# Optimization experiments

Hardware: AMD Instinct MI355X
Metric: run time of the kernel (lower is better)

Reference implementation:

```python
import jax, jax.numpy as jnp
import numpy as np

B, NPG = 128, 128          # graphs, nodes per graph
N = B * NPG                # total nodes
K = 16                     # kNN neighbors within cutoff
D = 256                    # embedding_depth
H, DH = 4, 32              # heads = num_layers, head dim = (D//2)//H
L = 4                      # num graph convolutions
NR = 50                    # num_radial
CUTOFF = 2.0
OUT = 3 + 100              # 3 + max_ntypes


def setup_inputs() -> dict:
    rng = np.random.default_rng(0)
    pos = rng.standard_normal((N, 3)).astype(np.float32)
    nbrs = np.zeros((N, K), np.int32)
    mask = np.zeros((N, K), np.float32)
    for g in range(B):  # per-graph kNN with radial cutoff (setup only, numpy)
        p = pos[g * NPG:(g + 1) * NPG]
        d2 = ((p[:, None, :] - p[None, :, :]) ** 2).sum(-1)
        np.fill_diagonal(d2, np.inf)
        idx = np.argsort(d2, axis=1)[:, :K]
        dk = np.sqrt(np.take_along_axis(d2, idx, 1))
        nbrs[g * NPG:(g + 1) * NPG] = idx + g * NPG
        mask[g * NPG:(g + 1) * NPG] = (dk <= CUTOFF).astype(np.float32)
    batch_idx = np.repeat(np.arange(B, dtype=np.int32), NPG)

    key = jax.random.key(0)
    ks = jax.random.split(key, 12)
    s = 0.02
    return {
        'encoding': jax.random.normal(ks[0], (B, D), jnp.float32),
        'pos': jnp.asarray(pos),
        'batch_idx': jnp.asarray(batch_idx),
        'neighbors': jnp.asarray(nbrs),
        'nbr_mask': jnp.asarray(mask),
        'W_in': jax.random.normal(ks[1], (D + 3, D), jnp.float32) * s,
        'b_in': jnp.zeros((D,), jnp.float32),
        'Wq': jax.random.normal(ks[2], (L, D, H * DH), jnp.float32) * s,
        'Wk': jax.random.normal(ks[3], (L, D, H * DH), jnp.float32) * s,
        'Wv': jax.random.normal(ks[4], (L, D, H * DH), jnp.float32) * s,
        'We': jax.random.normal(ks[5], (L, NR, H * DH), jnp.float32) * s,
        'Wo': jax.random.normal(ks[6], (L, H * DH, D), jnp.float32) * s,
        'bo': jnp.zeros((L, D), jnp.float32),
        'Wfc': jax.random.normal(ks[7], (L, D, D), jnp.float32) * s,
        'bfc': jnp.zeros((L, D), jnp.float32),
        'ln_g': jnp.ones((L, D), jnp.float32),
        'ln_b': jnp.zeros((L, D), jnp.float32),
        'W_out': jax.random.normal(ks[8], (D, OUT), jnp.float32) * s,
        'b_out': jnp.zeros((OUT,), jnp.float32),
    }


def reference(encoding, pos, batch_idx, neighbors, nbr_mask,
              W_in, b_in, Wq, Wk, Wv, We, Wo, bo, Wfc, bfc,
              ln_g, ln_b, W_out, b_out):
    # x = encoding.repeat_interleave(graph_sizes); x[:, 0] = 1
    x = encoding[batch_idx]                      # [N, D]
    x = x.at[:, 0].set(1.0)
    h = jnp.concatenate([x, pos], axis=-1) @ W_in + b_in   # concat pos, embed

    # gaussian radial basis of neighbor distances
    dvec = pos[neighbors] - pos[:, None, :]      # [N, K, 3]
    d = jnp.sqrt((dvec ** 2).sum(-1) + 1e-12)    # [N, K]
    centers = jnp.linspace(0.0, CUTOFF, NR)
    width = centers[1] - centers[0]
    rbf = jnp.exp(-0.5 * ((d[..., None] - centers) / width) ** 2)  # [N, K, NR]

    scale = 1.0 / jnp.sqrt(jnp.float32(DH))
    m = nbr_mask[..., None]                      # [N, K, 1]
    for l in range(L):                           # TransformerConv layers
        q = (h @ Wq[l]).reshape(N, H, DH)
        k = (h @ Wk[l]).reshape(N, H, DH)
        v = (h @ Wv[l]).reshape(N, H, DH)
        e = (rbf @ We[l]).reshape(N, K, H, DH)   # edge embedding
        kj = k[neighbors] + e                    # [N, K, H, DH]
        vj = v[neighbors] + e
        logits = jnp.einsum('nhd,nkhd->nkh', q, kj) * scale
        logits = jnp.where(m > 0, logits, -1e9)
        a = jax.nn.softmax(logits, axis=1) * m   # masked attention over K
        msg = jnp.einsum('nkh,nkhd->nhd', a, vj).reshape(N, H * DH)
        h = h + msg @ Wo[l] + bo[l]              # residual update
        mu = h.mean(-1, keepdims=True)
        var = h.var(-1, keepdims=True)
        h = ln_g[l] * (h - mu) / jnp.sqrt(var + 1e-5) + ln_b[l]
        h = jax.nn.gelu(h @ Wfc[l] + bfc[l])     # nodewise fc (1 layer)

    return h @ W_out + b_out                     # [N, 3 + max_ntypes]
```

## Files before the change

### kernel.cpp

```cpp
#include <hip/hip_runtime.h>
#include <hip/hip_bf16.h>
#include <math.h>

#define N_PTS 16384
#define NLAYER 4

typedef __attribute__((ext_vector_type(8))) short bfrag;
typedef __attribute__((ext_vector_type(4))) float f32x4;
typedef unsigned short ushort_t;
typedef unsigned int uint_t;

__device__ __forceinline__ ushort_t f2b(float f) {
  __hip_bfloat16 h = __float2bfloat16(f);
  return *reinterpret_cast<const ushort_t*>(&h);
}
__device__ __forceinline__ float b2f(ushort_t u) {
  union { uint_t i; float f; } c; c.i = ((uint_t)u) << 16; return c.f;
}
__device__ __forceinline__ float blo(uint_t u) {
  union { uint_t i; float f; } c; c.i = u << 16; return c.f;
}
__device__ __forceinline__ float bhi(uint_t u) {
  union { uint_t i; float f; } c; c.i = u & 0xffff0000u; return c.f;
}

__global__ __launch_bounds__(256) void base_kernel(
    const float* __restrict__ enc, const float* __restrict__ W_in,
    const float* __restrict__ b_in, float* __restrict__ base)
{
  int b = blockIdx.x, j = threadIdx.x;
  __shared__ float se[256];
  se[j] = enc[b * 256 + j];
  __syncthreads();
  float acc = b_in[j] + W_in[j];
  for (int i = 1; i < 256; ++i) acc += se[i] * W_in[i * 256 + j];
  base[b * 256 + j] = acc;
}

__global__ __launch_bounds__(256) void embed_kernel(
    const float* __restrict__ base, const int* __restrict__ batch_idx,
    const float* __restrict__ pos, const float* __restrict__ W_in,
    float* __restrict__ h, ushort_t* __restrict__ h_bf)
{
  int n = blockIdx.x, j = threadIdx.x;
  int b = batch_idx[n];
  float px = pos[n * 3 + 0], py = pos[n * 3 + 1], pz = pos[n * 3 + 2];
  float v = base[b * 256 + j]
      + px * W_in[256 * 256 + j] + py * W_in[257 * 256 + j] + pz * W_in[258 * 256 + j];
  h[(size_t)n * 256 + j] = v;
  h_bf[(size_t)n * 256 + j] = f2b(v);
}

__global__ __launch_bounds__(256) void prep_qkv(
    const float* __restrict__ Wq, const float* __restrict__ Wk,
    const float* __restrict__ Wv, const float* __restrict__ We,
    ushort_t* __restrict__ out)
{
  int idx = blockIdx.x * 256 + threadIdx.x;
  int l = idx / (640 * 256);
  int rem = idx - l * (640 * 256);
  int j = rem >> 8, k = rem & 255;
  float v = 0.f;
  if (j < 128) v = Wq[((size_t)l * 256 + k) * 128 + j];
  else if (j < 328) {
    int p = j - 128, hq = p / 50, r = p - hq * 50;
    const float* wq = &Wq[((size_t)l * 256 + k) * 128 + hq * 32];
    const float* we = &We[((size_t)l * 50 + r) * 128 + hq * 32];
#pragma unroll
    for (int d = 0; d < 32; ++d) v += wq[d] * we[d];
  } else if (j < 456) v = Wk[((size_t)l * 256 + k) * 128 + (j - 328)];
  else if (j < 584) v = Wv[((size_t)l * 256 + k) * 128 + (j - 456)];
  out[idx] = f2b(v);
}

__global__ __launch_bounds__(256) void prep_bcat(
    const float* __restrict__ We, const float* __restrict__ Wo, ushort_t* __restrict__ out)
{
  int idx = blockIdx.x * 256 + threadIdx.x;
  int l = idx / (256 * 384);
  int rem = idx - l * (256 * 384);
  int j = rem / 384, k2 = rem - j * 384;
  float v = 0.f;
  if (k2 < 128) v = Wo[((size_t)l * 128 + k2) * 256 + j];
  else if (k2 < 328) {
    int p = k2 - 128, hq = p / 50, r = p - hq * 50;
    const float* we = &We[((size_t)l * 50 + r) * 128 + hq * 32];
    const float* wo = &Wo[((size_t)l * 128 + hq * 32) * 256 + j];
#pragma unroll
    for (int d = 0; d < 32; ++d) v += we[d] * wo[(size_t)d * 256];
  }
  out[idx] = f2b(v);
}

__global__ __launch_bounds__(256) void prep_wfc(
    const float* __restrict__ Wfc, ushort_t* __restrict__ out)
{
  int idx = blockIdx.x * 256 + threadIdx.x;
  int l = idx >> 16, rem = idx & 65535;
  int j = rem >> 8, k = rem & 255;
  out[idx] = f2b(Wfc[((size_t)l * 256 + k) * 256 + j]);
}

__global__ __launch_bounds__(256) void prep_wout(
    const float* __restrict__ W_out, ushort_t* __restrict__ out)
{
  int idx = blockIdx.x * 256 + threadIdx.x;
  int j = idx >> 8, k = idx & 255;
  out[idx] = (j < 103) ? f2b(W_out[(size_t)k * 103 + j]) : (ushort_t)0;
}

template<int MODE>
__global__ __launch_bounds__(256, 3) void fused_layer(
    const ushort_t* __restrict__ A0,
    const ushort_t* __restrict__ BcT,
    const float* __restrict__ bo,
    float* __restrict__ h,
    const float* __restrict__ lg, const float* __restrict__ lb,
    const ushort_t* __restrict__ WfT,
    const float* __restrict__ bfc,
    const ushort_t* __restrict__ W3T,
    const float* __restrict__ b3,
    ushort_t* __restrict__ qext_b, ushort_t* __restrict__ kvb,
    float* __restrict__ outF)
{
  __shared__ __align__(16) ushort_t sA[32 * 392];
  __shared__ __align__(16) ushort_t sH[32 * 264];
  __shared__ float pS[4][32], pSS[4][32];

  const int tid = threadIdx.x;
  const int lane = tid & 63, w = tid >> 6;
  const int l15 = lane & 15, l4 = lane >> 4;
  const int m0 = blockIdx.x * 32;

  if constexpr (MODE != 2) {
    for (int i = tid; i < 32 * 44; i += 256) {
      int r = i / 44, c8 = i - r * 44;
      *(uint4*)(&sA[r * 392 + c8 * 8]) =
          *(const uint4*)(A0 + (size_t)(m0 + r) * 352 + c8 * 8);
    }
    __syncthreads();

    const int c_0 = w * 64 + l15, c_1 = c_0 + 16, c_2 = c_0 + 32, c_3 = c_0 + 48;

    f32x4 acc[2][4];
#pragma unroll
    for (int m = 0; m < 2; ++m)
#pragma unroll
      for (int nn = 0; nn < 4; ++nn) acc[m][nn] = (f32x4){0.f, 0.f, 0.f, 0.f};
    {
      const ushort_t* bp0 = BcT + (size_t)(c_0) * 384 + l4 * 8;
      const ushort_t* bp1 = BcT + (size_t)(c_1) * 384 + l4 * 8;
      const ushort_t* bp2 = BcT + (size_t)(c_2) * 384 + l4 * 8;
      const ushort_t* bp3 = BcT + (size_t)(c_3) * 384 + l4 * 8;
#pragma unroll
      for (int k0 = 0; k0 < 352; k0 += 32) {
        bfrag a0 = *(const bfrag*)(sA + l15 * 392 + k0 + l4 * 8);
        bfrag a1 = *(const bfrag*)(sA + (16 + l15) * 392 + k0 + l4 * 8);
        bfrag b0 = *(const bfrag*)(bp0 + k0);
        bfrag b1 = *(const bfrag*)(bp1 + k0);
        bfrag b2 = *(const bfrag*)(bp2 + k0);
        bfrag b3v = *(const bfrag*)(bp3 + k0);
        __builtin_amdgcn_s_setprio(1);
        acc[0][0] = __builtin_amdgcn_mfma_f32_16x16x32_bf16(a0, b0, acc[0][0], 0, 0, 0);
        acc[0][1] = __builtin_amdgcn_mfma_f32_16x16x32_bf16(a0, b1, acc[0][1], 0, 0, 0);
        acc[0][2] = __builtin_amdgcn_mfma_f32_16x16x32_bf16(a0, b2, acc[0][2], 0, 0, 0);
        acc[0][3] = __builtin_amdgcn_mfma_f32_16x16x32_bf16(a0, b3v, acc[0][3], 0, 0, 0);
        acc[1][0] = __builtin_amdgcn_mfma_f32_16x16x32_bf16(a1, b0, acc[1][0], 0, 0, 0);
        acc[1][1] = __builtin_amdgcn_mfma_f32_16x16x32_bf16(a1, b1, acc[1][1], 0, 0, 0);
        acc[1][2] = __builtin_amdgcn_mfma_f32_16x16x32_bf16(a1, b2, acc[1][2], 0, 0, 0);
        acc[1][3] = __builtin_amdgcn_mfma_f32_16x16x32_bf16(a1, b3v, acc[1][3], 0, 0, 0);
        __builtin_amdgcn_s_setprio(0);
      }
    }

    {
      const float bo_[4] = {bo[c_0], bo[c_1], bo[c_2], bo[c_3]};
#pragma unroll
      for (int m = 0; m < 2; ++m)
#pragma unroll
        for (int i = 0; i < 4; ++i) {
          const int rl = m * 16 + l4 * 4 + i;
          const size_t r = (size_t)(m0 + rl);
          float x0 = acc[m][0][i] + bo_[0] + h[r * 256 + c_0];
          float x1 = acc[m][1][i] + bo_[1] + h[r * 256 + c_1];
          float x2 = acc[m][2][i] + bo_[2] + h[r * 256 + c_2];
          float x3 = acc[m][3][i] + bo_[3] + h[r * 256 + c_3];
          acc[m][0][i] = x0; acc[m][1][i] = x1;
          acc[m][2][i] = x2; acc[m][3][i] = x3;
          float s = x0 + x1 + x2 + x3;
          float ss = x0 * x0 + x1 * x1 + x2 * x2 + x3 * x3;
          s += __shfl_xor(s, 1, 64); ss += __shfl_xor(ss, 1, 64);
          s += __shfl_xor(s, 2, 64); ss += __shfl_xor(ss, 2, 64);
          s += __shfl_xor(s, 4, 64); ss += __shfl_xor(ss, 4, 64);
          s += __shfl_xor(s, 8, 64); ss += __shfl_xor(ss, 8, 64);
          if (l15 == 0) { pS[w][rl] = s; pSS[w][rl] = ss; }
        }
    }
    __syncthreads();
    {
      const float lg_[4] = {lg[c_0], lg[c_1], lg[c_2], lg[c_3]};
      const float lb_[4] = {lb[c_0], lb[c_1], lb[c_2], lb[c_3]};
#pragma unroll
      for (int m = 0; m < 2; ++m)
#pragma unroll
        for (int i = 0; i < 4; ++i) {
          const int rl = m * 16 + l4 * 4 + i;
          float s = pS[0][rl] + pS[1][rl] + pS[2][rl] + pS[3][rl];
          float ss = pSS[0][rl] + pSS[1][rl] + pSS[2][rl] + pSS[3][rl];
          float mu = s * (1.f / 256.f);
          float var = ss * (1.f / 256.f) - mu * mu;
          float inv = 1.0f / sqrtf(var + 1e-5f);
          sH[rl * 264 + c_0] = f2b(lg_[0] * (acc[m][0][i] - mu) * inv + lb_[0]);
          sH[rl * 264 + c_1] = f2b(lg_[1] * (acc[m][1][i] - mu) * inv + lb_[1]);
          sH[rl * 264 + c_2] = f2b(lg_[2] * (acc[m][2][i] - mu) * inv + lb_[2]);
          sH[rl * 264 + c_3] = f2b(lg_[3] * (acc[m][3][i] - mu) * inv + lb_[3]);
        }
    }
    __syncthreads();

#pragma unroll
    for (int m = 0; m < 2; ++m)
#pragma unroll
      for (int nn = 0; nn < 4; ++nn) acc[m][nn] = (f32x4){0.f, 0.f, 0.f, 0.f};
    {
      const ushort_t* bp0 = WfT + (size_t)(c_0) * 256 + l4 * 8;
      const ushort_t* bp1 = WfT + (size_t)(c_1) * 256 + l4 * 8;
      const ushort_t* bp2 = WfT + (size_t)(c_2) * 256 + l4 * 8;
      const ushort_t* bp3 = WfT + (size_t)(c_3) * 256 + l4 * 8;
#pragma unroll
      for (int k0 = 0; k0 < 256; k0 += 32) {
        bfrag a0 = *(const bfrag*)(sH + l15 * 264 + k0 + l4 * 8);
        bfrag a1 = *(const bfrag*)(sH + (16 + l15) * 264 + k0 + l4 * 8);
        bfrag b0 = *(const bfrag*)(bp0 + k0);
        bfrag b1 = *(const bfrag*)(bp1 + k0);
        bfrag b2 = *(const bfrag*)(bp2 + k0);
        bfrag b3v = *(const bfrag*)(bp3 + k0);
        __builtin_amdgcn_s_setprio(1);
        acc[0][0] = __builtin_amdgcn_mfma_f32_16x16x32_bf16(a0, b0, acc[0][0], 0, 0, 0);
        acc[0][1] = __builtin_amdgcn_mfma_f32_16x16x32_bf16(a0, b1, acc[0][1], 0, 0, 0);
        acc[0][2] = __builtin_amdgcn_mfma_f32_16x16x32_bf16(a0, b2, acc[0][2], 0, 0, 0);
        acc[0][3] = __builtin_amdgcn_mfma_f32_16x16x32_bf16(a0, b3v, acc[0][3], 0, 0, 0);
        acc[1][0] = __builtin_amdgcn_mfma_f32_16x16x32_bf16(a1, b0, acc[1][0], 0, 0, 0);
        acc[1][1] = __builtin_amdgcn_mfma_f32_16x16x32_bf16(a1, b1, acc[1][1], 0, 0, 0);
        acc[1][2] = __builtin_amdgcn_mfma_f32_16x16x32_bf16(a1, b2, acc[1][2], 0, 0, 0);
        acc[1][3] = __builtin_amdgcn_mfma_f32_16x16x32_bf16(a1, b3v, acc[1][3], 0, 0, 0);
        __builtin_amdgcn_s_setprio(0);
      }
    }

    {
      const float bf_[4] = {bfc[c_0], bfc[c_1], bfc[c_2], bfc[c_3]};
      const int cc[4] = {c_0, c_1, c_2, c_3};
#pragma unroll
      for (int m = 0; m < 2; ++m)
#pragma unroll
        for (int i = 0; i < 4; ++i) {
          const int rl = m * 16 + l4 * 4 + i;
          const size_t r = (size_t)(m0 + rl);
#pragma unroll
          for (int nn = 0; nn < 4; ++nn) {
            float x = acc[m][nn][i] + bf_[nn];
            float t = tanhf(0.7978845608028654f * (x + 0.044715f * x * x * x));
            float gl = 0.5f * x * (1.f + t);
            h[r * 256 + cc[nn]] = gl;
            sA[rl * 264 + cc[nn]] = f2b(gl);
          }
        }
    }
    __syncthreads();
  } else {
    for (int i = tid; i < 32 * 32; i += 256) {
      int r = i >> 5, c8 = i & 31;
      *(uint4*)(&sA[r * 264 + c8 * 8]) =
          *(const uint4*)(A0 + (size_t)(m0 + r) * 256 + c8 * 8);
    }
    __syncthreads();
  }

  const int NPAN = (MODE == 1) ? 2 : 10;
  const int WCOL = (MODE == 1) ? 32 : 160;
  for (int p = 0; p < NPAN; ++p) {
    const int cb = w * WCOL + p * 16;
    const int c = cb + l15;
    const ushort_t* bp = W3T + (size_t)c * 256 + l4 * 8;
    f32x4 aA[2], aB[2];
    aA[0] = (f32x4){0.f, 0.f, 0.f, 0.f}; aA[1] = aA[0];
    aB[0] = aA[0]; aB[1] = aA[0];
#pragma unroll
    for (int k0 = 0; k0 < 128; k0 += 32) {
      bfrag a0 = *(const bfrag*)(sA + l15 * 264 + k0 + l4 * 8);
      bfrag a1 = *(const bfrag*)(sA + (16 + l15) * 264 + k0 + l4 * 8);
      bfrag b0 = *(const bfrag*)(bp + k0);
      __builtin_amdgcn_s_setprio(1);
      aA[0] = __builtin_amdgcn_mfma_f32_16x16x32_bf16(a0, b0, aA[0], 0, 0, 0);
      aA[1] = __builtin_amdgcn_mfma_f32_16x16x32_bf16(a1, b0, aA[1], 0, 0, 0);
      __builtin_amdgcn_s_setprio(0);
    }
#pragma unroll
    for (int k0 = 128; k0 < 256; k0 += 32) {
      bfrag a0 = *(const bfrag*)(sA + l15 * 264 + k0 + l4 * 8);
      bfrag a1 = *(const bfrag*)(sA + (16 + l15) * 264 + k0 + l4 * 8);
      bfrag b0 = *(const bfrag*)(bp + k0);
      __builtin_amdgcn_s_setprio(1);
      aB[0] = __builtin_amdgcn_mfma_f32_16x16x32_bf16(a0, b0, aB[0], 0, 0, 0);
      aB[1] = __builtin_amdgcn_mfma_f32_16x16x32_bf16(a1, b0, aB[1], 0, 0, 0);
      __builtin_amdgcn_s_setprio(0);
    }
#pragma unroll
    for (int m = 0; m < 2; ++m)
#pragma unroll
      for (int i = 0; i < 4; ++i) {
        const size_t r = (size_t)(m0 + m * 16 + l4 * 4 + i);
        float v = aA[m][i] + aB[m][i];
        if constexpr (MODE == 1) {
          if (c < 103) outF[r * 103 + c] = v + b3[c];
        } else {
          if (c < 328) qext_b[r * 352 + c] = f2b(v);
          else if (c < 584) kvb[r * 256 + (c - 328)] = f2b(v);
        }
      }
  }
}

__global__ __launch_bounds__(256) void attn_kernel(
    const ushort_t* __restrict__ qext, const ushort_t* __restrict__ kvb,
    const float* __restrict__ pos, const int* __restrict__ nbrs,
    const float* __restrict__ mask, ushort_t* __restrict__ Amsg)
{
  __shared__ __align__(16) ushort_t sQ[4][128];
  __shared__ __align__(16) float    sQE[4][4][52];
  __shared__ __align__(16) ushort_t sRbf[4][16][52];
  __shared__ float sA[4][64];
  __shared__ float sD[4][16];
  __shared__ float sMk[4][16];
  __shared__ int   sNb[4][16];

  const int tid = threadIdx.x;
  const int lane = tid & 63, w = tid >> 6;
  const int g = blockIdx.x & 127, q4 = blockIdx.x >> 7;
  const int kk = lane >> 2, hh = lane & 3;

  for (int it = 0; it < 4; ++it) {
    const int n = g * 128 + q4 * 16 + w * 4 + it;
    if (lane < 16) {
      int nb = nbrs[n * 16 + lane];
      sNb[w][lane] = nb;
      sMk[w][lane] = mask[n * 16 + lane];
      float dx = pos[nb * 3 + 0] - pos[n * 3 + 0];
      float dy = pos[nb * 3 + 1] - pos[n * 3 + 1];
      float dz = pos[nb * 3 + 2] - pos[n * 3 + 2];
      sD[w][lane] = sqrtf(dx * dx + dy * dy + dz * dz + 1e-12f);
      sRbf[w][lane][50] = 0; sRbf[w][lane][51] = 0;
      *(uint4*)(&sQ[w][lane * 8]) = *(const uint4*)(qext + (size_t)n * 352 + lane * 8);
    }
    if (lane < 50) {
      uint2 u = *(const uint2*)(qext + (size_t)n * 352 + 128 + lane * 4);
      int p = lane * 4;
#pragma unroll
      for (int e = 0; e < 4; ++e) {
        ushort_t bb = ((const ushort_t*)&u)[e];
        int pp = p + e, h2 = pp / 50, r = pp - h2 * 50;
        sQE[w][h2][r] = b2f(bb);
      }
    }
    if (lane < 8) sQE[w][lane >> 1][50 + (lane & 1)] = 0.f;
    {
      int kk2 = lane & 15;
      float dk = sD[w][kk2];
      int r0 = lane >> 4;
#pragma unroll
      for (int j = 0; j < 13; ++j) {
        int r = r0 + j * 4;
        if (r < 50) {
          float t = (dk - (2.f / 49.f) * (float)r) * 24.5f;
          sRbf[w][kk2][r] = f2b(__expf(-0.5f * t * t));
        }
      }
    }
    const int nb = sNb[w][kk];
    const ushort_t* krow = kvb + (size_t)nb * 256 + hh * 32;
    float qk = 0.f;
#pragma unroll
    for (int c8 = 0; c8 < 4; ++c8) {
      uint4 kv4 = *(const uint4*)(krow + c8 * 8);
      const uint_t* q4p = (const uint_t*)(&sQ[w][hh * 32 + c8 * 8]);
      uint_t qa = q4p[0], qb = q4p[1], qc = q4p[2], qd = q4p[3];
      qk += blo(qa) * blo(kv4.x) + bhi(qa) * bhi(kv4.x)
          + blo(qb) * blo(kv4.y) + bhi(qb) * bhi(kv4.y)
          + blo(qc) * blo(kv4.z) + bhi(qc) * bhi(kv4.z)
          + blo(qd) * blo(kv4.w) + bhi(qd) * bhi(kv4.w);
    }
    float qe = 0.f;
#pragma unroll
    for (int c = 0; c < 13; ++c) {
      float4 qv = *(const float4*)(&sQE[w][hh][c * 4]);
      uint2 rv = *(const uint2*)(&sRbf[w][kk][c * 4]);
      qe += qv.x * blo(rv.x) + qv.y * bhi(rv.x)
          + qv.z * blo(rv.y) + qv.w * bhi(rv.y);
    }
    float lg = 0.17677669529663687f * (qk + qe);
    lg = (sMk[w][kk] > 0.f) ? lg : -1e9f;

    float mx = lg;
#pragma unroll
    for (int off = 4; off < 64; off <<= 1) mx = fmaxf(mx, __shfl_xor(mx, off, 64));
    float ex = __expf(lg - mx);
    float sm = ex;
#pragma unroll
    for (int off = 4; off < 64; off <<= 1) sm += __shfl_xor(sm, off, 64);
    sA[w][kk * 4 + hh] = ex / sm * sMk[w][kk];

    if (lane < 50) {
      float r0 = 0.f, r1 = 0.f, r2 = 0.f, r3 = 0.f;
#pragma unroll
      for (int k2 = 0; k2 < 16; ++k2) {
        float rb = b2f(sRbf[w][k2][lane]);
        r0 += sA[w][k2 * 4 + 0] * rb;
        r1 += sA[w][k2 * 4 + 1] * rb;
        r2 += sA[w][k2 * 4 + 2] * rb;
        r3 += sA[w][k2 * 4 + 3] * rb;
      }
      Amsg[(size_t)n * 352 + 128 + 0 * 50 + lane] = f2b(r0);
      Amsg[(size_t)n * 352 + 128 + 1 * 50 + lane] = f2b(r1);
      Amsg[(size_t)n * 352 + 128 + 2 * 50 + lane] = f2b(r2);
      Amsg[(size_t)n * 352 + 128 + 3 * 50 + lane] = f2b(r3);
    }
    {
      const int h2 = lane >> 4;
      float m0v = 0.f, m1v = 0.f;
#pragma unroll
      for (int k2 = 0; k2 < 16; ++k2) {
        int nb2 = sNb[w][k2];
        uint_t vv = *(const uint_t*)(kvb + (size_t)nb2 * 256 + 128 + lane * 2);
        float a = sA[w][k2 * 4 + h2];
        m0v += a * blo(vv);
        m1v += a * bhi(vv);
      }
      uint_t o = (uint_t)f2b(m0v) | ((uint_t)f2b(m1v) << 16);
      *(uint_t*)(&Amsg[(size_t)n * 352 + lane * 2]) = o;
    }
    if (lane < 24) Amsg[(size_t)n * 352 + 328 + lane] = 0;
  }
}

extern "C" void kernel_launch(void* const* d_in, const int* in_sizes, int n_in,
                              void* d_out, int out_size, void* d_ws, size_t ws_size,
                              hipStream_t stream) {
  const float* enc    = (const float*)d_in[0];
  const float* pos    = (const float*)d_in[1];
  const int*   bidx   = (const int*)  d_in[2];
  const int*   nbrs   = (const int*)  d_in[3];
  const float* mask   = (const float*)d_in[4];
  const float* W_in   = (const float*)d_in[5];
  const float* b_in   = (const float*)d_in[6];
  const float* Wq     = (const float*)d_in[7];
  const float* Wk     = (const float*)d_in[8];
  const float* Wv     = (const float*)d_in[9];
  const float* We     = (const float*)d_in[10];
  const float* Wo     = (const float*)d_in[11];
  const float* bo     = (const float*)d_in[12];
  const float* Wfc    = (const float*)d_in[13];
  const float* bfc    = (const float*)d_in[14];
  const float* ln_g   = (const float*)d_in[15];
  const float* ln_b   = (const float*)d_in[16];
  const float* W_out  = (const float*)d_in[17];
  const float* b_out  = (const float*)d_in[18];
  float* out = (float*)d_out;

  const int N = N_PTS;
  float* ws = (float*)d_ws;
  float*    h      = ws;
  ushort_t* qext_b = (ushort_t*)(h + (size_t)N * 256);
  ushort_t* kvb    = qext_b + (size_t)N * 352;
  ushort_t* h_bf   = kvb + (size_t)N * 256;
  ushort_t* Amsg   = h_bf + (size_t)N * 256;
  float*    base   = (float*)(Amsg + (size_t)N * 352);
  ushort_t* WqkvT  = (ushort_t*)(base + 128 * 256);
  ushort_t* BcT    = WqkvT + 4 * 640 * 256;
  ushort_t* WfT    = BcT  + 4 * 256 * 384;
  ushort_t* WoT    = WfT  + 4 * 256 * 256;

  base_kernel<<<128, 256, 0, stream>>>(enc, W_in, b_in, base);
  embed_kernel<<<N, 256, 0, stream>>>(base, bidx, pos, W_in, h, h_bf);
  prep_qkv<<<(4 * 640 * 256) / 256, 256, 0, stream>>>(Wq, Wk, Wv, We, WqkvT);
  prep_bcat<<<(4 * 256 * 384) / 256, 256, 0, stream>>>(We, Wo, BcT);
  prep_wfc<<<(4 * 256 * 256) / 256, 256, 0, stream>>>(Wfc, WfT);
  prep_wout<<<(128 * 256) / 256, 256, 0, stream>>>(W_out, WoT);

  fused_layer<2><<<N / 32, 256, 0, stream>>>(
      h_bf, nullptr, nullptr, nullptr, nullptr, nullptr, nullptr, nullptr,
      WqkvT, nullptr, qext_b, kvb, nullptr);

  for (int l = 0; l < NLAYER; ++l) {
    const ushort_t* BcT_l = BcT + (size_t)l * 256 * 384;
    const ushort_t* WfT_l = WfT + (size_t)l * 256 * 256;
    const float* bo_l  = bo  + (size_t)l * 256;
    const float* bfc_l = bfc + (size_t)l * 256;
    const float* lg_l  = ln_g + (size_t)l * 256;
    const float* lb_l  = ln_b + (size_t)l * 256;

    attn_kernel<<<1024, 256, 0, stream>>>(qext_b, kvb, pos, nbrs, mask, Amsg);

    if (l < NLAYER - 1) {
      const ushort_t* Wqkv_next = WqkvT + (size_t)(l + 1) * 640 * 256;
      fused_layer<0><<<N / 32, 256, 0, stream>>>(
          Amsg, BcT_l, bo_l, h, lg_l, lb_l, WfT_l, bfc_l,
          Wqkv_next, nullptr, qext_b, kvb, nullptr);
    } else {
      fused_layer<1><<<N / 32, 256, 0, stream>>>(
          Amsg, BcT_l, bo_l, h, lg_l, lb_l, WfT_l, bfc_l,
          WoT, b_out, nullptr, nullptr, out);
    }
  }
}
```

Baseline: 387.0 us.

## Retile fused layer warps to 2x2 row/column split with register-prefetched operands

Reorganizes the fused layer so each warp owns 16 rows by 128 columns, reading the A operand straight from global memory instead of staging it in shared memory. B fragments are double-buffered in registers so the next k-step's loads overlap the current MFMAs. The QKV/output projection panel loop becomes a strided tile loop over 16-column tiles with two tiles in flight. Occupancy hint drops from 3 to 2 blocks per CU to make room for the larger register footprint, and the output weight prep is widened to 144 rows to cover the padded tile count.

Result: slower. 469.7 us (+21.4%).

```diff
diff --git a/kernel.cpp b/kernel.cpp
--- a/kernel.cpp
+++ b/kernel.cpp
@@ -23,6 +23,8 @@
 __device__ __forceinline__ float bhi(uint_t u) {
   union { uint_t i; float f; } c; c.i = u & 0xffff0000u; return c.f;
 }
+
+#define MFMA16(a, b, c) __builtin_amdgcn_mfma_f32_16x16x32_bf16((a), (b), (c), 0, 0, 0)
 
 __global__ __launch_bounds__(256) void base_kernel(
     const float* __restrict__ enc, const float* __restrict__ W_in,
@@ -105,12 +107,13 @@
     const float* __restrict__ W_out, ushort_t* __restrict__ out)
 {
   int idx = blockIdx.x * 256 + threadIdx.x;
+  if (idx >= 144 * 256) return;
   int j = idx >> 8, k = idx & 255;
   out[idx] = (j < 103) ? f2b(W_out[(size_t)k * 103 + j]) : (ushort_t)0;
 }
 
 template<int MODE>
-__global__ __launch_bounds__(256, 3) void fused_layer(
+__global__ __launch_bounds__(256, 2) void fused_layer(
     const ushort_t* __restrict__ A0,
     const ushort_t* __restrict__ BcT,
     const float* __restrict__ bo,
@@ -123,202 +126,189 @@
     ushort_t* __restrict__ qext_b, ushort_t* __restrict__ kvb,
     float* __restrict__ outF)
 {
-  __shared__ __align__(16) ushort_t sA[32 * 392];
   __shared__ __align__(16) ushort_t sH[32 * 264];
-  __shared__ float pS[4][32], pSS[4][32];
+  __shared__ __align__(16) ushort_t sG[32 * 264];
+  __shared__ float pS[2][32], pSS[2][32];
 
   const int tid = threadIdx.x;
   const int lane = tid & 63, w = tid >> 6;
+  const int rh = w >> 1, ch = w & 1;
   const int l15 = lane & 15, l4 = lane >> 4;
   const int m0 = blockIdx.x * 32;
+  const int arow = rh * 16 + l15;
 
   if constexpr (MODE != 2) {
-    for (int i = tid; i < 32 * 44; i += 256) {
-      int r = i / 44, c8 = i - r * 44;
-      *(uint4*)(&sA[r * 392 + c8 * 8]) =
-          *(const uint4*)(A0 + (size_t)(m0 + r) * 352 + c8 * 8);
+    const int cbase = ch * 128;
+
+    f32x4 acc[8];
+#pragma unroll
+    for (int nt = 0; nt < 8; ++nt) acc[nt] = (f32x4){0.f, 0.f, 0.f, 0.f};
+    {
+      const ushort_t* ap = A0 + (size_t)(m0 + arow) * 352 + l4 * 8;
+      const ushort_t* bp[8];
+#pragma unroll
+      for (int nt = 0; nt < 8; ++nt)
+        bp[nt] = BcT + (size_t)(cbase + nt * 16 + l15) * 384 + l4 * 8;
+      bfrag aC = *(const bfrag*)ap;
+      bfrag bC[8];
+#pragma unroll
+      for (int nt = 0; nt < 8; ++nt) bC[nt] = *(const bfrag*)bp[nt];
+#pragma unroll
+      for (int ks = 0; ks < 11; ++ks) {
+        bfrag aN{}; bfrag bN[8];
+        if (ks < 10) {
+          aN = *(const bfrag*)(ap + (ks + 1) * 32);
+#pragma unroll
+          for (int nt = 0; nt < 8; ++nt) bN[nt] = *(const bfrag*)(bp[nt] + (ks + 1) * 32);
+        }
+        __builtin_amdgcn_s_setprio(1);
+#pragma unroll
+        for (int nt = 0; nt < 8; ++nt) acc[nt] = MFMA16(aC, bC[nt], acc[nt]);
+        __builtin_amdgcn_s_setprio(0);
+        if (ks < 10) {
+          aC = aN;
+#pragma unroll
+          for (int nt = 0; nt < 8; ++nt) bC[nt] = bN[nt];
+        }
+      }
+    }
+
+    {
+#pragma unroll
+      for (int i = 0; i < 4; ++i) {
+        const int rl = rh * 16 + l4 * 4 + i;
+        const size_t r = (size_t)(m0 + rl);
+        float s = 0.f, ss = 0.f;
+#pragma unroll
+        for (int nt = 0; nt < 8; ++nt) {
+          const int c = cbase + nt * 16 + l15;
+          float x = acc[nt][i] + bo[c] + h[r * 256 + c];
+          acc[nt][i] = x;
+          s += x; ss += x * x;
+        }
+        s += __shfl_xor(s, 1, 64); ss += __shfl_xor(ss, 1, 64);
+        s += __shfl_xor(s, 2, 64); ss += __shfl_xor(ss, 2, 64);
+        s += __shfl_xor(s, 4, 64); ss += __shfl_xor(ss, 4, 64);
+        s += __shfl_xor(s, 8, 64); ss += __shfl_xor(ss, 8, 64);
+        if (l15 == 0) { pS[ch][rl] = s; pSS[ch][rl] = ss; }
+      }
     }
     __syncthreads();
-
-    const int c_0 = w * 64 + l15, c_1 = c_0 + 16, c_2 = c_0 + 32, c_3 = c_0 + 48;
-
-    f32x4 acc[2][4];
-#pragma unroll
-    for (int m = 0; m < 2; ++m)
-#pragma unroll
-      for (int nn = 0; nn < 4; ++nn) acc[m][nn] = (f32x4){0.f, 0.f, 0.f, 0.f};
-    {
-      const ushort_t* bp0 = BcT + (size_t)(c_0) * 384 + l4 * 8;
-      const ushort_t* bp1 = BcT + (size_t)(c_1) * 384 + l4 * 8;
-      const ushort_t* bp2 = BcT + (size_t)(c_2) * 384 + l4 * 8;
-      const ushort_t* bp3 = BcT + (size_t)(c_3) * 384 + l4 * 8;
-#pragma unroll
-      for (int k0 = 0; k0 < 352; k0 += 32) {
-        bfrag a0 = *(const bfrag*)(sA + l15 * 392 + k0 + l4 * 8);
-        bfrag a1 = *(const bfrag*)(sA + (16 + l15) * 392 + k0 + l4 * 8);
-        bfrag b0 = *(const bfrag*)(bp0 + k0);
-        bfrag b1 = *(const bfrag*)(bp1 + k0);
-        bfrag b2 = *(const bfrag*)(bp2 + k0);
-        bfrag b3v = *(const bfrag*)(bp3 + k0);
+    {
+#pragma unroll
+      for (int i = 0; i < 4; ++i) {
+        const int rl = rh * 16 + l4 * 4 + i;
+        float s = pS[0][rl] + pS[1][rl];
+        float ss = pSS[0][rl] + pSS[1][rl];
+        float mu = s * (1.f / 256.f);
+        float var = ss * (1.f / 256.f) - mu * mu;
+        float inv = 1.0f / sqrtf(var + 1e-5f);
+#pragma unroll
+        for (int nt = 0; nt < 8; ++nt) {
+          const int c = cbase + nt * 16 + l15;
+          sH[rl * 264 + c] = f2b(lg[c] * (acc[nt][i] - mu) * inv + lb[c]);
+        }
+      }
+    }
+    __syncthreads();
+
+#pragma unroll
+    for (int nt = 0; nt < 8; ++nt) acc[nt] = (f32x4){0.f, 0.f, 0.f, 0.f};
+    {
+      const ushort_t* bp[8];
+#pragma unroll
+      for (int nt = 0; nt < 8; ++nt)
+        bp[nt] = WfT + (size_t)(cbase + nt * 16 + l15) * 256 + l4 * 8;
+      bfrag bC[8];
+#pragma unroll
+      for (int nt = 0; nt < 8; ++nt) bC[nt] = *(const bfrag*)bp[nt];
+#pragma unroll
+      for (int ks = 0; ks < 8; ++ks) {
+        bfrag bN[8];
+        if (ks < 7) {
+#pragma unroll
+          for (int nt = 0; nt < 8; ++nt) bN[nt] = *(const bfrag*)(bp[nt] + (ks + 1) * 32);
+        }
+        bfrag aC = *(const bfrag*)(sH + arow * 264 + ks * 32 + l4 * 8);
         __builtin_amdgcn_s_setprio(1);
-        acc[0][0] = __builtin_amdgcn_mfma_f32_16x16x32_bf16(a0, b0, acc[0][0], 0, 0, 0);
-        acc[0][1] = __builtin_amdgcn_mfma_f32_16x16x32_bf16(a0, b1, acc[0][1], 0, 0, 0);
-        acc[0][2] = __builtin_amdgcn_mfma_f32_16x16x32_bf16(a0, b2, acc[0][2], 0, 0, 0);
-        acc[0][3] = __builtin_amdgcn_mfma_f32_16x16x32_bf16(a0, b3v, acc[0][3], 0, 0, 0);
-        acc[1][0] = __builtin_amdgcn_mfma_f32_16x16x32_bf16(a1, b0, acc[1][0], 0, 0, 0);
-        acc[1][1] = __builtin_amdgcn_mfma_f32_16x16x32_bf16(a1, b1, acc[1][1], 0, 0, 0);
-        acc[1][2] = __builtin_amdgcn_mfma_f32_16x16x32_bf16(a1, b2, acc[1][2], 0, 0, 0);
-        acc[1][3] = __builtin_amdgcn_mfma_f32_16x16x32_bf16(a1, b3v, acc[1][3], 0, 0, 0);
+#pragma unroll
+        for (int nt = 0; nt < 8; ++nt) acc[nt] = MFMA16(aC, bC[nt], acc[nt]);
         __builtin_amdgcn_s_setprio(0);
-      }
-    }
-
-    {
-      const float bo_[4] = {bo[c_0], bo[c_1], bo[c_2], bo[c_3]};
-#pragma unroll
-      for (int m = 0; m < 2; ++m)
-#pragma unroll
-        for (int i = 0; i < 4; ++i) {
-          const int rl = m * 16 + l4 * 4 + i;
-          const size_t r = (size_t)(m0 + rl);
-          float x0 = acc[m][0][i] + bo_[0] + h[r * 256 + c_0];
-          float x1 = acc[m][1][i] + bo_[1] + h[r * 256 + c_1];
-          float x2 = acc[m][2][i] + bo_[2] + h[r * 256 + c_2];
-          float x3 = acc[m][3][i] + bo_[3] + h[r * 256 + c_3];
-          acc[m][0][i] = x0; acc[m][1][i] = x1;
-          acc[m][2][i] = x2; acc[m][3][i] = x3;
-          float s = x0 + x1 + x2 + x3;
-          float ss = x0 * x0 + x1 * x1 + x2 * x2 + x3 * x3;
-          s += __shfl_xor(s, 1, 64); ss += __shfl_xor(ss, 1, 64);
-          s += __shfl_xor(s, 2, 64); ss += __shfl_xor(ss, 2, 64);
-          s += __shfl_xor(s, 4, 64); ss += __shfl_xor(ss, 4, 64);
-          s += __shfl_xor(s, 8, 64); ss += __shfl_xor(ss, 8, 64);
-          if (l15 == 0) { pS[w][rl] = s; pSS[w][rl] = ss; }
-        }
-    }
-    __syncthreads();
-    {
-      const float lg_[4] = {lg[c_0], lg[c_1], lg[c_2], lg[c_3]};
-      const float lb_[4] = {lb[c_0], lb[c_1], lb[c_2], lb[c_3]};
-#pragma unroll
-      for (int m = 0; m < 2; ++m)
-#pragma unroll
-        for (int i = 0; i < 4; ++i) {
-          const int rl = m * 16 + l4 * 4 + i;
-          float s = pS[0][rl] + pS[1][rl] + pS[2][rl] + pS[3][rl];
-          float ss = pSS[0][rl] + pSS[1][rl] + pSS[2][rl] + pSS[3][rl];
-          float mu = s * (1.f / 256.f);
-          float var = ss * (1.f / 256.f) - mu * mu;
-          float inv = 1.0f / sqrtf(var + 1e-5f);
-          sH[rl * 264 + c_0] = f2b(lg_[0] * (acc[m][0][i] - mu) * inv + lb_[0]);
-          sH[rl * 264 + c_1] = f2b(lg_[1] * (acc[m][1][i] - mu) * inv + lb_[1]);
-          sH[rl * 264 + c_2] = f2b(lg_[2] * (acc[m][2][i] - mu) * inv + lb_[2]);
-          sH[rl * 264 + c_3] = f2b(lg_[3] * (acc[m][3][i] - mu) * inv + lb_[3]);
-        }
-    }
-    __syncthreads();
-
-#pragma unroll
-    for (int m = 0; m < 2; ++m)
-#pragma unroll
-      for (int nn = 0; nn < 4; ++nn) acc[m][nn] = (f32x4){0.f, 0.f, 0.f, 0.f};
-    {
-      const ushort_t* bp0 = WfT + (size_t)(c_0) * 256 + l4 * 8;
-      const ushort_t* bp1 = WfT + (size_t)(c_1) * 256 + l4 * 8;
-      const ushort_t* bp2 = WfT + (size_t)(c_2) * 256 + l4 * 8;
-      const ushort_t* bp3 = WfT + (size_t)(c_3) * 256 + l4 * 8;
-#pragma unroll
-      for (int k0 = 0; k0 < 256; k0 += 32) {
-        bfrag a0 = *(const bfrag*)(sH + l15 * 264 + k0 + l4 * 8);
-        bfrag a1 = *(const bfrag*)(sH + (16 + l15) * 264 + k0 + l4 * 8);
-        bfrag b0 = *(const bfrag*)(bp0 + k0);
-        bfrag b1 = *(const bfrag*)(bp1 + k0);
-        bfrag b2 = *(const bfrag*)(bp2 + k0);
-        bfrag b3v = *(const bfrag*)(bp3 + k0);
-        __builtin_amdgcn_s_setprio(1);
-        acc[0][0] = __builtin_amdgcn_mfma_f32_16x16x32_bf16(a0, b0, acc[0][0], 0, 0, 0);
-        acc[0][1] = __builtin_amdgcn_mfma_f32_16x16x32_bf16(a0, b1, acc[0][1], 0, 0, 0);
-        acc[0][2] = __builtin_amdgcn_mfma_f32_16x16x32_bf16(a0, b2, acc[0][2], 0, 0, 0);
-        acc[0][3] = __builtin_amdgcn_mfma_f32_16x16x32_bf16(a0, b3v, acc[0][3], 0, 0, 0);
-        acc[1][0] = __builtin_amdgcn_mfma_f32_16x16x32_bf16(a1, b0, acc[1][0], 0, 0, 0);
-        acc[1][1] = __builtin_amdgcn_mfma_f32_16x16x32_bf16(a1, b1, acc[1][1], 0, 0, 0);
-        acc[1][2] = __builtin_amdgcn_mfma_f32_16x16x32_bf16(a1, b2, acc[1][2], 0, 0, 0);
-        acc[1][3] = __builtin_amdgcn_mfma_f32_16x16x32_bf16(a1, b3v, acc[1][3], 0, 0, 0);
-        __builtin_amdgcn_s_setprio(0);
-      }
-    }
-
-    {
-      const float bf_[4] = {bfc[c_0], bfc[c_1], bfc[c_2], bfc[c_3]};
-      const int cc[4] = {c_0, c_1, c_2, c_3};
-#pragma unroll
-      for (int m = 0; m < 2; ++m)
-#pragma unroll
-        for (int i = 0; i < 4; ++i) {
-          const int rl = m * 16 + l4 * 4 + i;
-          const size_t r = (size_t)(m0 + rl);
-#pragma unroll
-          for (int nn = 0; nn < 4; ++nn) {
-            float x = acc[m][nn][i] + bf_[nn];
-            float t = tanhf(0.7978845608028654f * (x + 0.044715f * x * x * x));
-            float gl = 0.5f * x * (1.f + t);
-            h[r * 256 + cc[nn]] = gl;
-            sA[rl * 264 + cc[nn]] = f2b(gl);
-          }
-        }
+        if (ks < 7) {
+#pragma unroll
+          for (int nt = 0; nt < 8; ++nt) bC[nt] = bN[nt];
+        }
+      }
+    }
+
+    {
+#pragma unroll
+      for (int i = 0; i < 4; ++i) {
+        const int rl = rh * 16 + l4 * 4 + i;
+        const size_t r = (size_t)(m0 + rl);
+#pragma unroll
+        for (int nt = 0; nt < 8; ++nt) {
+          const int c = cbase + nt * 16 + l15;
+          float x = acc[nt][i] + bfc[c];
+          float t = tanhf(0.7978845608028654f * (x + 0.044715f * x * x * x));
+          float gl = 0.5f * x * (1.f + t);
+          h[r * 256 + c] = gl;
+          sG[rl * 264 + c] = f2b(gl);
+        }
+      }
     }
     __syncthreads();
   } else {
     for (int i = tid; i < 32 * 32; i += 256) {
       int r = i >> 5, c8 = i & 31;
-      *(uint4*)(&sA[r * 264 + c8 * 8]) =
+      *(uint4*)(&sG[r * 264 + c8 * 8]) =
           *(const uint4*)(A0 + (size_t)(m0 + r) * 256 + c8 * 8);
     }
     __syncthreads();
   }
 
-  const int NPAN = (MODE == 1) ? 2 : 10;
-  const int WCOL = (MODE == 1) ? 32 : 160;
-  for (int p = 0; p < NPAN; ++p) {
-    const int cb = w * WCOL + p * 16;
-    const int c = cb + l15;
-    const ushort_t* bp = W3T + (size_t)c * 256 + l4 * 8;
-    f32x4 aA[2], aB[2];
-    aA[0] = (f32x4){0.f, 0.f, 0.f, 0.f}; aA[1] = aA[0];
-    aB[0] = aA[0]; aB[1] = aA[0];
-#pragma unroll
-    for (int k0 = 0; k0 < 128; k0 += 32) {
-      bfrag a0 = *(const bfrag*)(sA + l15 * 264 + k0 + l4 * 8);
-      bfrag a1 = *(const bfrag*)(sA + (16 + l15) * 264 + k0 + l4 * 8);
-      bfrag b0 = *(const bfrag*)(bp + k0);
-      __builtin_amdgcn_s_setprio(1);
-      aA[0] = __builtin_amdgcn_mfma_f32_16x16x32_bf16(a0, b0, aA[0], 0, 0, 0);
-      aA[1] = __builtin_amdgcn_mfma_f32_16x16x32_bf16(a1, b0, aA[1], 0, 0, 0);
-      __builtin_amdgcn_s_setprio(0);
-    }
-#pragma unroll
-    for (int k0 = 128; k0 < 256; k0 += 32) {
-      bfrag a0 = *(const bfrag*)(sA + l15 * 264 + k0 + l4 * 8);
-      bfrag a1 = *(const bfrag*)(sA + (16 + l15) * 264 + k0 + l4 * 8);
-      bfrag b0 = *(const bfrag*)(bp + k0);
-      __builtin_amdgcn_s_setprio(1);
-      aB[0] = __builtin_amdgcn_mfma_f32_16x16x32_bf16(a0, b0, aB[0], 0, 0, 0);
-      aB[1] = __builtin_amdgcn_mfma_f32_16x16x32_bf16(a1, b0, aB[1], 0, 0, 0);
-      __builtin_amdgcn_s_setprio(0);
-    }
-#pragma unroll
-    for (int m = 0; m < 2; ++m)
+  {
+    const int NT = (MODE == 1) ? 7 : 37;
+    for (int t = ch; t < NT; t += 4) {
+      const int t2 = t + 2;
+      const bool has2 = (t2 < NT);
+      const int c0 = t * 16 + l15;
+      const int c1 = t2 * 16 + l15;
+      const ushort_t* wp0 = W3T + (size_t)c0 * 256 + l4 * 8;
+      const ushort_t* wp1 = W3T + (size_t)c1 * 256 + l4 * 8;
+      f32x4 a0v = (f32x4){0.f, 0.f, 0.f, 0.f};
+      f32x4 a1v = (f32x4){0.f, 0.f, 0.f, 0.f};
+#pragma unroll
+      for (int ks = 0; ks < 8; ++ks) {
+        bfrag av = *(const bfrag*)(sG + arow * 264 + ks * 32 + l4 * 8);
+        bfrag b0 = *(const bfrag*)(wp0 + ks * 32);
+        bfrag b1 = *(const bfrag*)(wp1 + ks * 32);
+        __builtin_amdgcn_s_setprio(1);
+        a0v = MFMA16(av, b0, a0v);
+        if (has2) a1v = MFMA16(av, b1, a1v);
+        __builtin_amdgcn_s_setprio(0);
+      }
 #pragma unroll
       for (int i = 0; i < 4; ++i) {
-        const size_t r = (size_t)(m0 + m * 16 + l4 * 4 + i);
-        float v = aA[m][i] + aB[m][i];
+        const size_t r = (size_t)(m0 + rh * 16 + l4 * 4 + i);
+        float v0 = a0v[i];
         if constexpr (MODE == 1) {
-          if (c < 103) outF[r * 103 + c] = v + b3[c];
+          if (c0 < 103) outF[r * 103 + c0] = v0 + b3[c0];
         } else {
-          if (c < 328) qext_b[r * 352 + c] = f2b(v);
-          else if (c < 584) kvb[r * 256 + (c - 328)] = f2b(v);
-        }
-      }
+          if (c0 < 328) qext_b[r * 352 + c0] = f2b(v0);
+          else if (c0 < 584) kvb[r * 256 + (c0 - 328)] = f2b(v0);
+        }
+        if (has2) {
+          float v1 = a1v[i];
+          if constexpr (MODE == 1) {
+            if (c1 < 103) outF[r * 103 + c1] = v1 + b3[c1];
+          } else {
+            if (c1 < 328) qext_b[r * 352 + c1] = f2b(v1);
+            else if (c1 < 584) kvb[r * 256 + (c1 - 328)] = f2b(v1);
+          }
+        }
+      }
+    }
   }
 }
 
@@ -485,7 +475,7 @@
   prep_qkv<<<(4 * 640 * 256) / 256, 256, 0, stream>>>(Wq, Wk, Wv, We, WqkvT);
   prep_bcat<<<(4 * 256 * 384) / 256, 256, 0, stream>>>(We, Wo, BcT);
   prep_wfc<<<(4 * 256 * 256) / 256, 256, 0, stream>>>(Wfc, WfT);
-  prep_wout<<<(128 * 256) / 256, 256, 0, stream>>>(W_out, WoT);
+  prep_wout<<<144, 256, 0, stream>>>(W_out, WoT);
 
   fused_layer<2><<<N / 32, 256, 0, stream>>>(
       h_bf, nullptr, nullptr, nullptr, nullptr, nullptr, nullptr, nullptr,
```
